# Performance work log

Hardware: AMD Instinct MI355X
Metric: run time of the kernel (lower is better)

The kernel has to match this reference:

```python
import jax, jax.numpy as jnp
import numpy as np

G, NPG, D_IN, HID, NH, DH = 128, 256, 15, 128, 8, 16
N = G * NPG
E = 1_048_576
NLAYERS = 3
EPS = 1e-5


def ln(x, g, b):
    m = x.mean(-1, keepdims=True)
    v = ((x - m) ** 2).mean(-1, keepdims=True)
    return (x - m) * jax.lax.rsqrt(v + EPS) * g + b


def gcn_conv(x, src, dst, W, b):
    # PyG GCNConv: add self-loops, symmetric deg^-1/2 normalization
    n = x.shape[0]
    h = x @ W  # [N, H]
    loop = jnp.arange(n)
    s = jnp.concatenate([src, loop])
    d = jnp.concatenate([dst, loop])
    deg = jnp.zeros((n,), x.dtype).at[d].add(1.0)  # >=1 due to self-loops
    dis = jax.lax.rsqrt(deg)
    coef = (dis[s] * dis[d])[:, None]
    return jnp.zeros_like(h).at[d].add(h[s] * coef) + b


def setup_inputs() -> dict:
    key = jax.random.key(0)
    ks = jax.random.split(key, 40)
    i = iter(range(40))

    def w(shape, scale=0.05):
        return jax.random.normal(ks[next(i)], shape, jnp.float32) * scale

    inp = {
        'x': jax.random.normal(ks[next(i)], (N, D_IN), jnp.float32),
        'edge_index': jax.random.randint(ks[next(i)], (2, E), 0, N),
        'batch': jnp.repeat(jnp.arange(G), NPG),  # 128 graphs x 256 nodes
        # input_proj: Linear + LayerNorm
        'W_in': w((D_IN, HID)), 'b_in': jnp.zeros((HID,)),
        'g_in': jnp.ones((HID,)), 'be_in': jnp.zeros((HID,)),
        # 3 GCNConv layers + LayerNorms (stacked)
        'Wc': w((NLAYERS, HID, HID)), 'bc': jnp.zeros((NLAYERS, HID)),
        'gn': jnp.ones((NLAYERS, HID)), 'bn': jnp.zeros((NLAYERS, HID)),
        # MultiheadAttention (in_proj split into q/k/v) + out_proj + post-LN
        'Wq': w((HID, HID)), 'bq': jnp.zeros((HID,)),
        'Wk': w((HID, HID)), 'bk': jnp.zeros((HID,)),
        'Wv': w((HID, HID)), 'bv': jnp.zeros((HID,)),
        'Wo': w((HID, HID)), 'bo': jnp.zeros((HID,)),
        'ga': jnp.ones((HID,)), 'ba': jnp.zeros((HID,)),
        # classifier: Linear(3H->H)+LN, Linear(H->H//2), Linear(H//2->2)
        'W1': w((3 * HID, HID)), 'b1': jnp.zeros((HID,)),
        'g1': jnp.ones((HID,)), 'beta1': jnp.zeros((HID,)),
        'W2': w((HID, HID // 2)), 'b2': jnp.zeros((HID // 2,)),
        'W3': w((HID // 2, 2)), 'b3': jnp.zeros((2,)),
    }
    return inp


def reference(x, edge_index, batch, W_in, b_in, g_in, be_in, Wc, bc, gn, bn,
              Wq, bq, Wk, bk, Wv, bv, Wo, bo, ga, ba,
              W1, b1, g1, beta1, W2, b2, W3, b3):
    src, dst = edge_index[0], edge_index[1]
    # input_proj (dropout is identity in eval)
    h = jax.nn.relu(ln(x @ W_in + b_in, g_in, be_in))
    # causal_graph_forward: GCN + LN + ReLU, residual for layers > 0
    for i in range(NLAYERS):
        h_res = h
        h = jax.nn.relu(ln(gcn_conv(h, src, dst, Wc[i], bc[i]), gn[i], bn[i]))
        if i > 0:
            h = h + h_res
    # per-graph MHA: equal-sized graphs -> block-diagonal == batched attention
    hg = h.reshape(G, NPG, HID)
    scale = 1.0 / np.sqrt(DH).astype(np.float32)
    q = (hg @ Wq.T + bq).reshape(G, NPG, NH, DH).transpose(0, 2, 1, 3)
    k = (hg @ Wk.T + bk).reshape(G, NPG, NH, DH).transpose(0, 2, 1, 3)
    v = (hg @ Wv.T + bv).reshape(G, NPG, NH, DH).transpose(0, 2, 1, 3)
    att = jax.nn.softmax(jnp.einsum('ghid,ghjd->ghij', q, k) * scale, axis=-1)
    o = jnp.einsum('ghij,ghjd->ghid', att, v).transpose(0, 2, 1, 3).reshape(G, NPG, HID)
    hg = ln(o @ Wo.T + bo + hg, ga, ba)
    # global mean/max/sum pooling per graph
    pooled = jnp.concatenate([hg.mean(1), hg.max(1), hg.sum(1)], axis=-1)  # [G, 3H]
    # classifier
    z = jax.nn.relu(ln(pooled @ W1 + b1, g1, beta1))
    z = jax.nn.relu(z @ W2 + b2)
    return z @ W3 + b3
```

## Files before the change

kernel.cpp:

```cpp
#include <hip/hip_runtime.h>
#include <hip/hip_bf16.h>

#define N_NODES 32768
#define E_EDGES 1048576
#define HID 128
#define G_GRAPHS 128
#define NPG 256
#define NH 8
#define DH 16
#define EPS 1e-5f
#define CHUNK 4096
#define BCAP 8192
#define BSTRIDE 16384

typedef __attribute__((ext_vector_type(4))) float f32x4;
typedef __attribute__((ext_vector_type(4))) short bf16x4;

static __device__ __forceinline__ unsigned short bfbits(float f) {
    return __builtin_bit_cast(unsigned short, __float2bfloat16(f));
}
static __device__ __forceinline__ float bf2f(unsigned short u) {
    return __builtin_bit_cast(float, (unsigned)u << 16);
}
static __device__ __forceinline__ float rdlanef(float v, int l) {
    return __builtin_bit_cast(float, __builtin_amdgcn_readlane(__builtin_bit_cast(int, v), l));
}

__device__ __forceinline__ void ln_stats128(float v, float& mean, float& istd, float* red) {
    float s = v, s2 = v * v;
#pragma unroll
    for (int off = 32; off; off >>= 1) { s += __shfl_xor(s, off); s2 += __shfl_xor(s2, off); }
    int w = threadIdx.x >> 6;
    if ((threadIdx.x & 63) == 0) { red[w * 2] = s; red[w * 2 + 1] = s2; }
    __syncthreads();
    float ts = red[0] + red[2], ts2 = red[1] + red[3];
    mean = ts * (1.f / 128.f);
    float var = ts2 * (1.f / 128.f) - mean * mean;
    istd = rsqrtf(var + EPS);
    __syncthreads();
}

__global__ __launch_bounds__(256) void bucket_scatter(const int* __restrict__ src,
                                                      const int* __restrict__ dst,
                                                      int* __restrict__ bucket_fill,
                                                      int* __restrict__ packed) {
    __shared__ int bcnt[256];
    __shared__ int lsc[256];
    __shared__ int delta[256];
    __shared__ int sorted[CHUNK];
    int tid = threadIdx.x;
    int base = blockIdx.x * CHUNK;
    int pk[16], bk[16], rk[16];
    bcnt[tid] = 0;
    __syncthreads();
#pragma unroll
    for (int j = 0; j < 16; j++) {
        int e = base + j * 256 + tid;
        int d = dst[e], s = src[e];
        pk[j] = (d << 15) | s;
        bk[j] = d >> 7;
    }
#pragma unroll
    for (int j = 0; j < 16; j++) rk[j] = atomicAdd(&bcnt[bk[j]], 1);
    __syncthreads();
    int cnt_t = bcnt[tid];
    lsc[tid] = cnt_t;
    __syncthreads();
    for (int off = 1; off < 256; off <<= 1) {
        int v = (tid >= off) ? lsc[tid - off] : 0;
        __syncthreads();
        lsc[tid] += v;
        __syncthreads();
    }
    int ls_t = lsc[tid] - cnt_t;
    __syncthreads();
    lsc[tid] = ls_t;
    int g = 0;
    if (cnt_t > 0) g = atomicAdd(&bucket_fill[tid], cnt_t);
    delta[tid] = tid * BSTRIDE + g - ls_t;
    __syncthreads();
#pragma unroll
    for (int j = 0; j < 16; j++) sorted[lsc[bk[j]] + rk[j]] = pk[j];
    __syncthreads();
    for (int i = tid; i < CHUNK; i += 256) {
        int u = sorted[i];
        int b2 = u >> 22;
        packed[delta[b2] + i] = u;
    }
}

__global__ __launch_bounds__(256) void csr_build(const int* __restrict__ bucket_fill,
                                                 const int* __restrict__ packed,
                                                 int* __restrict__ srcs,
                                                 int* __restrict__ row_ptr,
                                                 int* __restrict__ row_end,
                                                 float* __restrict__ dis) {
    __shared__ int ncnt[128];
    __shared__ int sc[128];
    __shared__ int fill[128];
    __shared__ int outl[BCAP];
    int b = blockIdx.x, tid = threadIdx.x;
    int c0 = b * BSTRIDE;
    int cnt = bucket_fill[b];
    if (tid < 128) ncnt[tid] = 0;
    __syncthreads();
    for (int i = tid; i < cnt; i += 256) {
        int u = packed[c0 + i];
        atomicAdd(&ncnt[(u >> 15) & 127], 1);
    }
    __syncthreads();
    int c = (tid < 128) ? ncnt[tid] : 0;
    if (tid < 128) sc[tid] = c;
    __syncthreads();
    for (int off = 1; off < 128; off <<= 1) {
        int v = (tid < 128 && tid >= off) ? sc[tid - off] : 0;
        __syncthreads();
        if (tid < 128) sc[tid] += v;
        __syncthreads();
    }
    if (tid < 128) {
        int ex = sc[tid] - c;
        fill[tid] = ex;
        int node = b * 128 + tid;
        row_ptr[node] = c0 + ex;
        row_end[node] = c0 + ex + c;
        dis[node] = rsqrtf((float)(c + 1));
    }
    __syncthreads();
    if (cnt <= BCAP) {
        for (int i = tid; i < cnt; i += 256) {
            int u = packed[c0 + i];
            int p = atomicAdd(&fill[(u >> 15) & 127], 1);
            outl[p] = u & 32767;
        }
        __syncthreads();
        for (int i = tid; i < cnt; i += 256) srcs[c0 + i] = outl[i];
    } else {
        for (int i = tid; i < cnt; i += 256) {
            int u = packed[c0 + i];
            int p = atomicAdd(&fill[(u >> 15) & 127], 1);
            srcs[c0 + p] = u & 32767;
        }
    }
}

__global__ __launch_bounds__(256) void prep_weights(const float* __restrict__ Wc,
                                                    const float* __restrict__ Wq,
                                                    const float* __restrict__ Wk,
                                                    const float* __restrict__ Wv,
                                                    const float* __restrict__ Wo,
                                                    const float* __restrict__ bq,
                                                    const float* __restrict__ bk,
                                                    const float* __restrict__ bv,
                                                    unsigned short* __restrict__ Wpk,
                                                    float* __restrict__ bT) {
    int m = blockIdx.y;
    int idx = blockIdx.x * 256 + threadIdx.x;
    int j = idx & 3, ln = (idx >> 2) & 63, kt = (idx >> 8) & 7, jt = (idx >> 11) & 7;
    int k = kt * 16 + (ln >> 4) * 4 + j;
    int col = jt * 16 + (ln & 15);
    float val;
    if (m < 3) val = Wc[m * 16384 + k * 128 + col];
    else {
        const float* W = (m == 3) ? Wq : (m == 4) ? Wk : (m == 5) ? Wv : Wo;
        val = W[col * 128 + k];
    }
    Wpk[m * 16384 + idx] = bfbits(val);
    if (m >= 3 && m < 6 && idx < 128) {
        const float* bs = (m == 3) ? bq : (m == 4) ? bk : bv;
        bT[(m - 3) * 128 + idx] = bs[idx];
    }
}

__global__ __launch_bounds__(128) void input_proj(const float* __restrict__ x,
                                                  const float* __restrict__ W,
                                                  const float* __restrict__ b,
                                                  const float* __restrict__ g,
                                                  const float* __restrict__ be,
                                                  unsigned short* __restrict__ h16) {
    int n = blockIdx.x, j = threadIdx.x;
    __shared__ float xs[15];
    __shared__ float red[4];
    if (j < 15) xs[j] = x[n * 15 + j];
    __syncthreads();
    float acc = b[j];
#pragma unroll
    for (int k = 0; k < 15; k++) acc += xs[k] * W[k * 128 + j];
    float m, is;
    ln_stats128(acc, m, is, red);
    float y = (acc - m) * is * g[j] + be[j];
    h16[(long)n * 128 + j] = bfbits(fmaxf(y, 0.f));
}

template <int MODE>
__device__ __forceinline__ void gemm_mfma_body(const unsigned short* __restrict__ in16,
                                               const unsigned short* __restrict__ Wpk,
                                               const float* __restrict__ bias,
                                               const unsigned short* __restrict__ resid16,
                                               const float* __restrict__ gamma,
                                               const float* __restrict__ beta,
                                               unsigned short* __restrict__ out16) {
    __shared__ unsigned short Ws[16384];
    __shared__ unsigned short Hs[64][136];
    int tid = threadIdx.x;
    long base = (long)blockIdx.x * 64;
    {
        const uint4* s4 = (const uint4*)Wpk;
        uint4* d4 = (uint4*)Ws;
        for (int i = tid; i < 2048; i += 256) d4[i] = s4[i];
        const unsigned short* hsrc = in16 + base * 128;
        for (int i = tid; i < 1024; i += 256) {
            int r = i >> 4, c8 = i & 15;
            *(uint4*)&Hs[r][c8 * 8] = *(const uint4*)&hsrc[r * 128 + c8 * 8];
        }
    }
    __syncthreads();
    int wv = tid >> 6, lane = tid & 63;
    int ql = lane & 15, qg = lane >> 4;
    f32x4 acc[8];
#pragma unroll
    for (int jt = 0; jt < 8; jt++) acc[jt] = (f32x4){0.f, 0.f, 0.f, 0.f};
#pragma unroll
    for (int kt = 0; kt < 8; kt++) {
        bf16x4 af = *(const bf16x4*)&Hs[wv * 16 + ql][kt * 16 + qg * 4];
#pragma unroll
        for (int jt = 0; jt < 8; jt++) {
            bf16x4 bf = *(const bf16x4*)&Ws[((jt * 8 + kt) * 64 + lane) * 4];
            acc[jt] = __builtin_amdgcn_mfma_f32_16x16x16bf16_1k(af, bf, acc[jt], 0, 0, 0);
        }
    }
    if (MODE >= 1) {
#pragma unroll
        for (int jt = 0; jt < 8; jt++) {
            float bv = bias[jt * 16 + ql];
#pragma unroll
            for (int r = 0; r < 4; r++) acc[jt][r] += bv;
        }
    }
    if (MODE == 2) {
#pragma unroll
        for (int jt = 0; jt < 8; jt++)
#pragma unroll
            for (int r = 0; r < 4; r++)
                acc[jt][r] += bf2f(resid16[(base + wv * 16 + qg * 4 + r) * 128 + jt * 16 + ql]);
        float s[4], s2[4], mean[4], istd[4];
#pragma unroll
        for (int r = 0; r < 4; r++) { s[r] = 0.f; s2[r] = 0.f; }
#pragma unroll
        for (int jt = 0; jt < 8; jt++)
#pragma unroll
            for (int r = 0; r < 4; r++) { float v = acc[jt][r]; s[r] += v; s2[r] += v * v; }
#pragma unroll
        for (int off = 1; off < 16; off <<= 1)
#pragma unroll
            for (int r = 0; r < 4; r++) {
                s[r] += __shfl_xor(s[r], off);
                s2[r] += __shfl_xor(s2[r], off);
            }
#pragma unroll
        for (int r = 0; r < 4; r++) {
            mean[r] = s[r] * (1.f / 128.f);
            float var = s2[r] * (1.f / 128.f) - mean[r] * mean[r];
            istd[r] = rsqrtf(var + EPS);
        }
#pragma unroll
        for (int jt = 0; jt < 8; jt++) {
            float gv = gamma[jt * 16 + ql], bev = beta[jt * 16 + ql];
#pragma unroll
            for (int r = 0; r < 4; r++)
                acc[jt][r] = (acc[jt][r] - mean[r]) * istd[r] * gv + bev;
        }
    }
#pragma unroll
    for (int jt = 0; jt < 8; jt++)
#pragma unroll
        for (int r = 0; r < 4; r++)
            Hs[wv * 16 + qg * 4 + r][jt * 16 + ql] = bfbits(acc[jt][r]);
#pragma unroll
    for (int p = 0; p < 4; p++) {
        int rl = p * 4 + qg;
        uint4 v = *(const uint4*)&Hs[wv * 16 + rl][ql * 8];
        *(uint4*)&out16[(base + wv * 16 + rl) * 128 + ql * 8] = v;
    }
}

template <int MODE>
__global__ __launch_bounds__(256) void gemm_mfma(const unsigned short* __restrict__ in16,
                                                 const unsigned short* __restrict__ Wpk,
                                                 const float* __restrict__ bias,
                                                 const unsigned short* __restrict__ resid16,
                                                 const float* __restrict__ gamma,
                                                 const float* __restrict__ beta,
                                                 unsigned short* __restrict__ out16) {
    gemm_mfma_body<MODE>(in16, Wpk, bias, resid16, gamma, beta, out16);
}

__global__ __launch_bounds__(256) void gemm_qkv(const unsigned short* __restrict__ in16,
                                                const unsigned short* __restrict__ Wpk,
                                                const float* __restrict__ bT,
                                                unsigned short* __restrict__ outb) {
    int y = blockIdx.y;
    gemm_mfma_body<1>(in16, Wpk + (3 + y) * 16384, bT + y * 128, nullptr, nullptr, nullptr,
                      outb + (long)y * N_NODES * 128);
}

__global__ __launch_bounds__(256) void gcn_agg(const unsigned short* __restrict__ hW,
                                               const int* __restrict__ row_ptr,
                                               const int* __restrict__ row_end,
                                               const int* __restrict__ srcs,
                                               const float* __restrict__ dis,
                                               const float* __restrict__ bias,
                                               const float* __restrict__ gamma,
                                               const float* __restrict__ beta,
                                               unsigned short* __restrict__ h16, int with_resid) {
    int wv = threadIdx.x >> 6, lane = threadIdx.x & 63;
    int n = blockIdx.x * 4 + wv;
    int r0 = row_ptr[n], r1 = row_end[n];
    float dn = dis[n];
    unsigned su = *(const unsigned*)&hW[(long)n * 128 + lane * 2];
    float dnn = dn * dn;
    float a0 = bf2f((unsigned short)(su & 0xffff)) * dnn;
    float a1 = bf2f((unsigned short)(su >> 16)) * dnn;
    for (int b = r0; b < r1; b += 64) {
        int cnt = min(64, r1 - b);
        int sv = n;
        float cv = 0.f;
        if (lane < cnt) {
            sv = srcs[b + lane];
            cv = dis[sv] * dn;
        }
        int cntR = (cnt + 15) & ~15;
        for (int j = 0; j < cntR; j += 16) {
            unsigned u[16];
#pragma unroll
            for (int t = 0; t < 16; t++) {
                int s = __builtin_amdgcn_readlane(sv, j + t);
                u[t] = *(const unsigned*)&hW[(long)s * 128 + lane * 2];
            }
#pragma unroll
            for (int t = 0; t < 16; t++) {
                float c = rdlanef(cv, j + t);
                a0 += bf2f((unsigned short)(u[t] & 0xffff)) * c;
                a1 += bf2f((unsigned short)(u[t] >> 16)) * c;
            }
        }
    }
    float2 bb = *(const float2*)&bias[lane * 2];
    a0 += bb.x;
    a1 += bb.y;
    float s = a0 + a1, s2 = a0 * a0 + a1 * a1;
#pragma unroll
    for (int off = 1; off < 64; off <<= 1) { s += __shfl_xor(s, off); s2 += __shfl_xor(s2, off); }
    float mean = s * (1.f / 128.f);
    float var = s2 * (1.f / 128.f) - mean * mean;
    float is = rsqrtf(var + EPS);
    float2 gg = *(const float2*)&gamma[lane * 2];
    float2 be2 = *(const float2*)&beta[lane * 2];
    float y0 = fmaxf((a0 - mean) * is * gg.x + be2.x, 0.f);
    float y1 = fmaxf((a1 - mean) * is * gg.y + be2.y, 0.f);
    if (with_resid) {
        unsigned ru = *(const unsigned*)&h16[(long)n * 128 + lane * 2];
        y0 += bf2f((unsigned short)(ru & 0xffff));
        y1 += bf2f((unsigned short)(ru >> 16));
    }
    unsigned outu = (unsigned)bfbits(y0) | ((unsigned)bfbits(y1) << 16);
    *(unsigned*)&h16[(long)n * 128 + lane * 2] = outu;
}

__global__ __launch_bounds__(256) void attention(const unsigned short* __restrict__ q16,
                                                 const unsigned short* __restrict__ k16,
                                                 const unsigned short* __restrict__ v16,
                                                 unsigned short* __restrict__ o16) {
    int g = blockIdx.x, hh = blockIdx.y;
    int tid = threadIdx.x;
    long gbase = ((long)g * NPG) * 128 + hh * 16;
    __shared__ unsigned short Ksh[256][24];
    __shared__ unsigned short Qsh[256][24];
    __shared__ unsigned short Vt[16][264];
    {
        const unsigned short* kp = k16 + gbase + (long)tid * 128;
        uint4 a = *(const uint4*)kp, b = *(const uint4*)(kp + 8);
        *(uint4*)&Ksh[tid][0] = a; *(uint4*)&Ksh[tid][8] = b;
        const unsigned short* qp = q16 + gbase + (long)tid * 128;
        uint4 c = *(const uint4*)qp, d = *(const uint4*)(qp + 8);
        *(uint4*)&Qsh[tid][0] = c; *(uint4*)&Qsh[tid][8] = d;
        const unsigned short* vp = v16 + gbase + (long)tid * 128;
#pragma unroll
        for (int dd = 0; dd < 16; dd++) Vt[dd][tid] = vp[dd];
    }
    __syncthreads();
    int wv = tid >> 6, lane = tid & 63;
    int qg = lane >> 4, ql = lane & 15;
    bf16x4 vfrag[16];
#pragma unroll
    for (int kt = 0; kt < 16; kt++)
        vfrag[kt] = *(const bf16x4*)&Vt[ql][kt * 16 + qg * 4];
    const float C = 0.36067376022224085f;
    for (int qi = 0; qi < 4; qi++) {
        int qt = wv * 4 + qi;
        bf16x4 qfrag = *(const bf16x4*)&Qsh[qt * 16 + ql][qg * 4];
        float lsum = 0.f;
        bf16x4 pb[16];
        f32x4 z4 = {0.f, 0.f, 0.f, 0.f};
#pragma unroll
        for (int kt = 0; kt < 16; kt++) {
            bf16x4 kfrag = *(const bf16x4*)&Ksh[kt * 16 + ql][qg * 4];
            f32x4 s4 = __builtin_amdgcn_mfma_f32_16x16x16bf16_1k(kfrag, qfrag, z4, 0, 0, 0);
            bf16x4 pbk;
#pragma unroll
            for (int r = 0; r < 4; r++) {
                float pv = exp2f(s4[r] * C);
                lsum += pv;
                pbk[r] = (short)bfbits(pv);
            }
            pb[kt] = pbk;
        }
        f32x4 oacc = {0.f, 0.f, 0.f, 0.f};
#pragma unroll
        for (int kt = 0; kt < 16; kt++)
            oacc = __builtin_amdgcn_mfma_f32_16x16x16bf16_1k(vfrag[kt], pb[kt], oacc, 0, 0, 0);
        lsum += __shfl_xor(lsum, 16);
        lsum += __shfl_xor(lsum, 32);
        float inv = 1.f / lsum;
        unsigned short* op = o16 + gbase + (long)(qt * 16 + ql) * 128 + 4 * qg;
        ushort4 st;
        st.x = bfbits(oacc[0] * inv);
        st.y = bfbits(oacc[1] * inv);
        st.z = bfbits(oacc[2] * inv);
        st.w = bfbits(oacc[3] * inv);
        *(ushort4*)op = st;
    }
}

__global__ __launch_bounds__(256) void pool_kernel(const unsigned short* __restrict__ hg,
                                                   float* __restrict__ pooled) {
    int g = blockIdx.x;
    int lane = threadIdx.x & 63, grp = threadIdx.x >> 6;
    __shared__ float ssum[4][128];
    __shared__ float smax[4][128];
    float s0 = 0.f, s1 = 0.f, m0 = -1e30f, m1 = -1e30f;
    for (int i = grp * 64; i < grp * 64 + 64; i++) {
        unsigned u = *(const unsigned*)&hg[((long)g * NPG + i) * 128 + lane * 2];
        float v0 = bf2f((unsigned short)(u & 0xffff));
        float v1 = bf2f((unsigned short)(u >> 16));
        s0 += v0; s1 += v1;
        m0 = fmaxf(m0, v0); m1 = fmaxf(m1, v1);
    }
    ssum[grp][lane * 2] = s0; ssum[grp][lane * 2 + 1] = s1;
    smax[grp][lane * 2] = m0; smax[grp][lane * 2 + 1] = m1;
    __syncthreads();
    if (grp == 0) {
        for (int jj = lane; jj < 128; jj += 64) {
            float ts = ssum[0][jj] + ssum[1][jj] + ssum[2][jj] + ssum[3][jj];
            float tm = fmaxf(fmaxf(smax[0][jj], smax[1][jj]), fmaxf(smax[2][jj], smax[3][jj]));
            pooled[g * 384 + jj] = ts * (1.f / 256.f);
            pooled[g * 384 + 128 + jj] = tm;
            pooled[g * 384 + 256 + jj] = ts;
        }
    }
}

__global__ __launch_bounds__(128) void classifier(const float* __restrict__ pooled,
                                                  const float* __restrict__ W1, const float* __restrict__ b1,
                                                  const float* __restrict__ g1, const float* __restrict__ be1,
                                                  const float* __restrict__ W2, const float* __restrict__ b2,
                                                  const float* __restrict__ W3, const float* __restrict__ b3,
                                                  float* __restrict__ out) {
    int g = blockIdx.x, j = threadIdx.x;
    __shared__ float pl[384];
    __shared__ float z1s[128];
    __shared__ float z2s[64];
    __shared__ float red[4];
    for (int i = j; i < 384; i += 128) pl[i] = pooled[g * 384 + i];
    __syncthreads();
    float acc = b1[j];
    for (int kk = 0; kk < 384; kk++) acc += pl[kk] * W1[kk * 128 + j];
    float m, is;
    ln_stats128(acc, m, is, red);
    float y = fmaxf((acc - m) * is * g1[j] + be1[j], 0.f);
    z1s[j] = y;
    __syncthreads();
    if (j < 64) {
        float a2 = b2[j];
        for (int kk = 0; kk < 128; kk++) a2 += z1s[kk] * W2[kk * 64 + j];
        z2s[j] = fmaxf(a2, 0.f);
    }
    __syncthreads();
    if (j < 64) {
        float vv = z2s[j];
        float p0 = vv * W3[j * 2];
        float p1 = vv * W3[j * 2 + 1];
#pragma unroll
        for (int off = 32; off; off >>= 1) { p0 += __shfl_xor(p0, off); p1 += __shfl_xor(p1, off); }
        if (j == 0) {
            out[g * 2] = p0 + b3[0];
            out[g * 2 + 1] = p1 + b3[1];
        }
    }
}

extern "C" void kernel_launch(void* const* d_in, const int* in_sizes, int n_in,
                              void* d_out, int out_size, void* d_ws, size_t ws_size,
                              hipStream_t stream) {
    const float* x = (const float*)d_in[0];
    const int* ei = (const int*)d_in[1];
    const float* W_in = (const float*)d_in[3];
    const float* b_in = (const float*)d_in[4];
    const float* g_in = (const float*)d_in[5];
    const float* be_in = (const float*)d_in[6];
    const float* Wc = (const float*)d_in[7];
    const float* bc = (const float*)d_in[8];
    const float* gn = (const float*)d_in[9];
    const float* bn = (const float*)d_in[10];
    const float* Wq = (const float*)d_in[11];
    const float* bq = (const float*)d_in[12];
    const float* Wk = (const float*)d_in[13];
    const float* bk = (const float*)d_in[14];
    const float* Wv = (const float*)d_in[15];
    const float* bv = (const float*)d_in[16];
    const float* Wo = (const float*)d_in[17];
    const float* bo = (const float*)d_in[18];
    const float* ga = (const float*)d_in[19];
    const float* ba = (const float*)d_in[20];
    const float* W1 = (const float*)d_in[21];
    const float* b1 = (const float*)d_in[22];
    const float* g1 = (const float*)d_in[23];
    const float* be1 = (const float*)d_in[24];
    const float* W2 = (const float*)d_in[25];
    const float* b2 = (const float*)d_in[26];
    const float* W3 = (const float*)d_in[27];
    const float* b3 = (const float*)d_in[28];
    float* out = (float*)d_out;

    const long NF = (long)N_NODES * 128;
    unsigned char* wsb = (unsigned char*)d_ws;
    const size_t MB = 1 << 20;
    unsigned short* h16 = (unsigned short*)(wsb);
    unsigned short* hw16 = (unsigned short*)(wsb + 8 * MB);
    unsigned short* qkv16 = (unsigned short*)(wsb + 16 * MB);
    unsigned short* o16 = (unsigned short*)(wsb + 40 * MB);
    unsigned short* hg16 = (unsigned short*)(wsb + 48 * MB);
    unsigned short* Wpk = (unsigned short*)(wsb + 56 * MB);
    int* srcs = (int*)(wsb + 57 * MB);
    int* packed = (int*)(wsb + 73 * MB);
    int* row_ptr = (int*)(wsb + 89 * MB);
    int* row_end = (int*)(wsb + 90 * MB);
    float* dis = (float*)(wsb + 91 * MB);
    float* bT = (float*)(wsb + 92 * MB);
    float* pooled = (float*)(wsb + 92 * MB + 4096);
    int* bucket_fill = (int*)(wsb + 93 * MB);

    const int* e_src = ei;
    const int* e_dst = ei + E_EDGES;

    hipMemsetAsync(bucket_fill, 0, 256 * sizeof(int), stream);
    prep_weights<<<dim3(64, 7), 256, 0, stream>>>(Wc, Wq, Wk, Wv, Wo, bq, bk, bv, Wpk, bT);
    bucket_scatter<<<E_EDGES / CHUNK, 256, 0, stream>>>(e_src, e_dst, bucket_fill, packed);
    csr_build<<<256, 256, 0, stream>>>(bucket_fill, packed, srcs, row_ptr, row_end, dis);

    input_proj<<<N_NODES, 128, 0, stream>>>(x, W_in, b_in, g_in, be_in, h16);

    for (int i = 0; i < 3; i++) {
        gemm_mfma<0><<<N_NODES / 64, 256, 0, stream>>>(h16, Wpk + i * 16384, nullptr, nullptr,
                                                       nullptr, nullptr, hw16);
        gcn_agg<<<N_NODES / 4, 256, 0, stream>>>(hw16, row_ptr, row_end, srcs, dis, bc + i * 128,
                                                 gn + i * 128, bn + i * 128, h16, i > 0);
    }

    gemm_qkv<<<dim3(N_NODES / 64, 3), 256, 0, stream>>>(h16, Wpk, bT, qkv16);

    attention<<<dim3(G_GRAPHS, NH), 256, 0, stream>>>(qkv16, qkv16 + NF, qkv16 + 2 * NF, o16);

    gemm_mfma<2><<<N_NODES / 64, 256, 0, stream>>>(o16, Wpk + 6 * 16384, bo, h16, ga, ba, hg16);

    pool_kernel<<<G_GRAPHS, 256, 0, stream>>>(hg16, pooled);
    classifier<<<G_GRAPHS, 128, 0, stream>>>(pooled, W1, b1, g1, be1, W2, b2, W3, b3, out);
}
```

Measured before the change: 352.6 us.

## Split GCN aggregation into two feature-half passes over planar hW layout

The GEMM now writes hW as two planes of 64 features each, so a node row is 128 bytes instead of 256. Aggregation runs as two kernels, one per feature half, with each wave gathering two edges at once using its upper and lower 32-lane halves. The first pass stores its partial result and LayerNorm sums, and the second pass finishes the normalization. The aim is a smaller gather working set per pass, which should fit better in cache, plus better lane use. The cost is an extra kernel launch, reading the CSR twice, an intermediate buffer round trip, and bf16 rounding of the first half before its statistics are computed.

```diff
diff --git a/kernel.cpp b/kernel.cpp
--- a/kernel.cpp
+++ b/kernel.cpp
@@ -192,7 +192,7 @@
     h16[(long)n * 128 + j] = bfbits(fmaxf(y, 0.f));
 }
 
-template <int MODE>
+template <int MODE, int PLANES>
 __device__ __forceinline__ void gemm_mfma_body(const unsigned short* __restrict__ in16,
                                                const unsigned short* __restrict__ Wpk,
                                                const float* __restrict__ bias,
@@ -280,11 +280,18 @@
     for (int p = 0; p < 4; p++) {
         int rl = p * 4 + qg;
         uint4 v = *(const uint4*)&Hs[wv * 16 + rl][ql * 8];
-        *(uint4*)&out16[(base + wv * 16 + rl) * 128 + ql * 8] = v;
-    }
-}
-
-template <int MODE>
+        if (PLANES) {
+            long row = base + wv * 16 + rl;
+            long off = (ql < 8) ? (row * 64 + ql * 8)
+                                : ((long)N_NODES * 64 + row * 64 + (ql - 8) * 8);
+            *(uint4*)&out16[off] = v;
+        } else {
+            *(uint4*)&out16[(base + wv * 16 + rl) * 128 + ql * 8] = v;
+        }
+    }
+}
+
+template <int MODE, int PLANES>
 __global__ __launch_bounds__(256) void gemm_mfma(const unsigned short* __restrict__ in16,
                                                  const unsigned short* __restrict__ Wpk,
                                                  const float* __restrict__ bias,
@@ -292,7 +299,7 @@
                                                  const float* __restrict__ gamma,
                                                  const float* __restrict__ beta,
                                                  unsigned short* __restrict__ out16) {
-    gemm_mfma_body<MODE>(in16, Wpk, bias, resid16, gamma, beta, out16);
+    gemm_mfma_body<MODE, PLANES>(in16, Wpk, bias, resid16, gamma, beta, out16);
 }
 
 __global__ __launch_bounds__(256) void gemm_qkv(const unsigned short* __restrict__ in16,
@@ -300,71 +307,165 @@
                                                 const float* __restrict__ bT,
                                                 unsigned short* __restrict__ outb) {
     int y = blockIdx.y;
-    gemm_mfma_body<1>(in16, Wpk + (3 + y) * 16384, bT + y * 128, nullptr, nullptr, nullptr,
-                      outb + (long)y * N_NODES * 128);
-}
-
-__global__ __launch_bounds__(256) void gcn_agg(const unsigned short* __restrict__ hW,
-                                               const int* __restrict__ row_ptr,
-                                               const int* __restrict__ row_end,
-                                               const int* __restrict__ srcs,
-                                               const float* __restrict__ dis,
-                                               const float* __restrict__ bias,
-                                               const float* __restrict__ gamma,
-                                               const float* __restrict__ beta,
-                                               unsigned short* __restrict__ h16, int with_resid) {
+    gemm_mfma_body<1, 0>(in16, Wpk + (3 + y) * 16384, bT + y * 128, nullptr, nullptr, nullptr,
+                         outb + (long)y * N_NODES * 128);
+}
+
+__global__ __launch_bounds__(256) void gcn_pass0(const unsigned short* __restrict__ plane,
+                                                 const int* __restrict__ row_ptr,
+                                                 const int* __restrict__ row_end,
+                                                 const int* __restrict__ srcs,
+                                                 const float* __restrict__ dis,
+                                                 const float* __restrict__ bias,
+                                                 unsigned short* __restrict__ agg,
+                                                 float2* __restrict__ psum) {
     int wv = threadIdx.x >> 6, lane = threadIdx.x & 63;
+    int l32 = lane & 31, hi = lane >> 5;
     int n = blockIdx.x * 4 + wv;
     int r0 = row_ptr[n], r1 = row_end[n];
     float dn = dis[n];
-    unsigned su = *(const unsigned*)&hW[(long)n * 128 + lane * 2];
-    float dnn = dn * dn;
-    float a0 = bf2f((unsigned short)(su & 0xffff)) * dnn;
-    float a1 = bf2f((unsigned short)(su >> 16)) * dnn;
+    float a0, a1;
+    {
+        unsigned su = *(const unsigned*)&plane[(long)n * 64 + l32 * 2];
+        float dh = dn * dn * 0.5f;
+        a0 = bf2f((unsigned short)(su & 0xffff)) * dh;
+        a1 = bf2f((unsigned short)(su >> 16)) * dh;
+    }
     for (int b = r0; b < r1; b += 64) {
         int cnt = min(64, r1 - b);
         int sv = n;
         float cv = 0.f;
         if (lane < cnt) {
-            sv = srcs[b + lane];
+            sv = __builtin_nontemporal_load(&srcs[b + lane]);
             cv = dis[sv] * dn;
         }
-        int cntR = (cnt + 15) & ~15;
-        for (int j = 0; j < cntR; j += 16) {
+        int pairs = (cnt + 1) >> 1;
+        int pR = (pairs + 15) & ~15;
+        for (int j = 0; j < pR; j += 16) {
             unsigned u[16];
 #pragma unroll
             for (int t = 0; t < 16; t++) {
-                int s = __builtin_amdgcn_readlane(sv, j + t);
-                u[t] = *(const unsigned*)&hW[(long)s * 128 + lane * 2];
+                int e = 2 * (j + t);
+                int sA = __builtin_amdgcn_readlane(sv, e);
+                int sB = __builtin_amdgcn_readlane(sv, e + 1);
+                int ss = hi ? sB : sA;
+                u[t] = *(const unsigned*)&plane[(long)ss * 64 + l32 * 2];
             }
 #pragma unroll
             for (int t = 0; t < 16; t++) {
-                float c = rdlanef(cv, j + t);
+                int e = 2 * (j + t);
+                float c = hi ? rdlanef(cv, e + 1) : rdlanef(cv, e);
                 a0 += bf2f((unsigned short)(u[t] & 0xffff)) * c;
                 a1 += bf2f((unsigned short)(u[t] >> 16)) * c;
             }
         }
     }
-    float2 bb = *(const float2*)&bias[lane * 2];
-    a0 += bb.x;
-    a1 += bb.y;
+    a0 += __shfl_xor(a0, 32);
+    a1 += __shfl_xor(a1, 32);
+    float2 bb = *(const float2*)&bias[l32 * 2];
+    a0 += bb.x; a1 += bb.y;
+    unsigned short u0 = bfbits(a0), u1 = bfbits(a1);
+    float q0 = bf2f(u0), q1 = bf2f(u1);
+    float s = q0 + q1, s2 = q0 * q0 + q1 * q1;
+#pragma unroll
+    for (int off = 1; off < 32; off <<= 1) { s += __shfl_xor(s, off); s2 += __shfl_xor(s2, off); }
+    if (lane == 0) psum[n] = make_float2(s, s2);
+    if (hi == 0) {
+        unsigned pk = (unsigned)u0 | ((unsigned)u1 << 16);
+        __builtin_nontemporal_store(pk, (unsigned*)&agg[(long)n * 64 + l32 * 2]);
+    }
+}
+
+__global__ __launch_bounds__(256) void gcn_pass1(const unsigned short* __restrict__ plane,
+                                                 const int* __restrict__ row_ptr,
+                                                 const int* __restrict__ row_end,
+                                                 const int* __restrict__ srcs,
+                                                 const float* __restrict__ dis,
+                                                 const float* __restrict__ bias,
+                                                 const float* __restrict__ gamma,
+                                                 const float* __restrict__ beta,
+                                                 const unsigned short* __restrict__ agg,
+                                                 const float2* __restrict__ psum,
+                                                 unsigned short* __restrict__ h16,
+                                                 int with_resid) {
+    int wv = threadIdx.x >> 6, lane = threadIdx.x & 63;
+    int l32 = lane & 31, hi = lane >> 5;
+    int n = blockIdx.x * 4 + wv;
+    int r0 = row_ptr[n], r1 = row_end[n];
+    float dn = dis[n];
+    float a0, a1;
+    {
+        unsigned su = *(const unsigned*)&plane[(long)n * 64 + l32 * 2];
+        float dh = dn * dn * 0.5f;
+        a0 = bf2f((unsigned short)(su & 0xffff)) * dh;
+        a1 = bf2f((unsigned short)(su >> 16)) * dh;
+    }
+    for (int b = r0; b < r1; b += 64) {
+        int cnt = min(64, r1 - b);
+        int sv = n;
+        float cv = 0.f;
+        if (lane < cnt) {
+            sv = __builtin_nontemporal_load(&srcs[b + lane]);
+            cv = dis[sv] * dn;
+        }
+        int pairs = (cnt + 1) >> 1;
+        int pR = (pairs + 15) & ~15;
+        for (int j = 0; j < pR; j += 16) {
+            unsigned u[16];
+#pragma unroll
+            for (int t = 0; t < 16; t++) {
+                int e = 2 * (j + t);
+                int sA = __builtin_amdgcn_readlane(sv, e);
+                int sB = __builtin_amdgcn_readlane(sv, e + 1);
+                int ss = hi ? sB : sA;
+                u[t] = *(const unsigned*)&plane[(long)ss * 64 + l32 * 2];
+            }
+#pragma unroll
+            for (int t = 0; t < 16; t++) {
+                int e = 2 * (j + t);
+                float c = hi ? rdlanef(cv, e + 1) : rdlanef(cv, e);
+                a0 += bf2f((unsigned short)(u[t] & 0xffff)) * c;
+                a1 += bf2f((unsigned short)(u[t] >> 16)) * c;
+            }
+        }
+    }
+    a0 += __shfl_xor(a0, 32);
+    a1 += __shfl_xor(a1, 32);
+    float2 bb = *(const float2*)&bias[64 + l32 * 2];
+    a0 += bb.x; a1 += bb.y;
     float s = a0 + a1, s2 = a0 * a0 + a1 * a1;
 #pragma unroll
-    for (int off = 1; off < 64; off <<= 1) { s += __shfl_xor(s, off); s2 += __shfl_xor(s2, off); }
-    float mean = s * (1.f / 128.f);
-    float var = s2 * (1.f / 128.f) - mean * mean;
+    for (int off = 1; off < 32; off <<= 1) { s += __shfl_xor(s, off); s2 += __shfl_xor(s2, off); }
+    float2 ps = psum[n];
+    float st = s + ps.x, s2t = s2 + ps.y;
+    float mean = st * (1.f / 128.f);
+    float var = s2t * (1.f / 128.f) - mean * mean;
     float is = rsqrtf(var + EPS);
-    float2 gg = *(const float2*)&gamma[lane * 2];
-    float2 be2 = *(const float2*)&beta[lane * 2];
-    float y0 = fmaxf((a0 - mean) * is * gg.x + be2.x, 0.f);
-    float y1 = fmaxf((a1 - mean) * is * gg.y + be2.y, 0.f);
-    if (with_resid) {
-        unsigned ru = *(const unsigned*)&h16[(long)n * 128 + lane * 2];
-        y0 += bf2f((unsigned short)(ru & 0xffff));
-        y1 += bf2f((unsigned short)(ru >> 16));
-    }
-    unsigned outu = (unsigned)bfbits(y0) | ((unsigned)bfbits(y1) << 16);
-    *(unsigned*)&h16[(long)n * 128 + lane * 2] = outu;
+    if (hi == 0) {
+        float2 gg1 = *(const float2*)&gamma[64 + l32 * 2];
+        float2 be1 = *(const float2*)&beta[64 + l32 * 2];
+        float y2 = fmaxf((a0 - mean) * is * gg1.x + be1.x, 0.f);
+        float y3 = fmaxf((a1 - mean) * is * gg1.y + be1.y, 0.f);
+        unsigned ua = __builtin_nontemporal_load((const unsigned*)&agg[(long)n * 64 + l32 * 2]);
+        float v0 = bf2f((unsigned short)(ua & 0xffff));
+        float v1 = bf2f((unsigned short)(ua >> 16));
+        float2 gg0 = *(const float2*)&gamma[l32 * 2];
+        float2 be0 = *(const float2*)&beta[l32 * 2];
+        float y0 = fmaxf((v0 - mean) * is * gg0.x + be0.x, 0.f);
+        float y1 = fmaxf((v1 - mean) * is * gg0.y + be0.y, 0.f);
+        if (with_resid) {
+            unsigned rA = *(const unsigned*)&h16[(long)n * 128 + l32 * 2];
+            unsigned rB = *(const unsigned*)&h16[(long)n * 128 + 64 + l32 * 2];
+            y0 += bf2f((unsigned short)(rA & 0xffff));
+            y1 += bf2f((unsigned short)(rA >> 16));
+            y2 += bf2f((unsigned short)(rB & 0xffff));
+            y3 += bf2f((unsigned short)(rB >> 16));
+        }
+        unsigned o0 = (unsigned)bfbits(y0) | ((unsigned)bfbits(y1) << 16);
+        unsigned o1 = (unsigned)bfbits(y2) | ((unsigned)bfbits(y3) << 16);
+        __builtin_nontemporal_store(o0, (unsigned*)&h16[(long)n * 128 + l32 * 2]);
+        __builtin_nontemporal_store(o1, (unsigned*)&h16[(long)n * 128 + 64 + l32 * 2]);
+    }
 }
 
 __global__ __launch_bounds__(256) void attention(const unsigned short* __restrict__ q16,
@@ -533,16 +634,19 @@
     float* out = (float*)d_out;
 
     const long NF = (long)N_NODES * 128;
+    const long NF64 = (long)N_NODES * 64;
     unsigned char* wsb = (unsigned char*)d_ws;
     const size_t MB = 1 << 20;
     unsigned short* h16 = (unsigned short*)(wsb);
-    unsigned short* hw16 = (unsigned short*)(wsb + 8 * MB);
+    unsigned short* hwp = (unsigned short*)(wsb + 8 * MB);
     unsigned short* qkv16 = (unsigned short*)(wsb + 16 * MB);
     unsigned short* o16 = (unsigned short*)(wsb + 40 * MB);
     unsigned short* hg16 = (unsigned short*)(wsb + 48 * MB);
     unsigned short* Wpk = (unsigned short*)(wsb + 56 * MB);
     int* srcs = (int*)(wsb + 57 * MB);
     int* packed = (int*)(wsb + 73 * MB);
+    unsigned short* agg = (unsigned short*)(wsb + 73 * MB);
+    float2* psum = (float2*)(wsb + 78 * MB);
     int* row_ptr = (int*)(wsb + 89 * MB);
     int* row_end = (int*)(wsb + 90 * MB);
     float* dis = (float*)(wsb + 91 * MB);
@@ -561,17 +665,20 @@
     input_proj<<<N_NODES, 128, 0, stream>>>(x, W_in, b_in, g_in, be_in, h16);
 
     for (int i = 0; i < 3; i++) {
-        gemm_mfma<0><<<N_NODES / 64, 256, 0, stream>>>(h16, Wpk + i * 16384, nullptr, nullptr,
-                                                       nullptr, nullptr, hw16);
-        gcn_agg<<<N_NODES / 4, 256, 0, stream>>>(hw16, row_ptr, row_end, srcs, dis, bc + i * 128,
-                                                 gn + i * 128, bn + i * 128, h16, i > 0);
+        gemm_mfma<0, 1><<<N_NODES / 64, 256, 0, stream>>>(h16, Wpk + i * 16384, nullptr, nullptr,
+                                                          nullptr, nullptr, hwp);
+        gcn_pass0<<<N_NODES / 4, 256, 0, stream>>>(hwp, row_ptr, row_end, srcs, dis,
+                                                   bc + i * 128, agg, psum);
+        gcn_pass1<<<N_NODES / 4, 256, 0, stream>>>(hwp + NF64, row_ptr, row_end, srcs, dis,
+                                                   bc + i * 128, gn + i * 128, bn + i * 128,
+                                                   agg, psum, h16, i > 0);
     }
 
     gemm_qkv<<<dim3(N_NODES / 64, 3), 256, 0, stream>>>(h16, Wpk, bT, qkv16);
 
     attention<<<dim3(G_GRAPHS, NH), 256, 0, stream>>>(qkv16, qkv16 + NF, qkv16 + 2 * NF, o16);
 
-    gemm_mfma<2><<<N_NODES / 64, 256, 0, stream>>>(o16, Wpk + 6 * 16384, bo, h16, ga, ba, hg16);
+    gemm_mfma<2, 0><<<N_NODES / 64, 256, 0, stream>>>(o16, Wpk + 6 * 16384, bo, h16, ga, ba, hg16);
 
     pool_kernel<<<G_GRAPHS, 256, 0, stream>>>(hg16, pooled);
     classifier<<<G_GRAPHS, 128, 0, stream>>>(pooled, W1, b1, g1, be1, W2, b2, W3, b3, out);
```

Measured after the change: 465.2 us. 1.32x slower.
